# Performance work log

Measured on AMD Instinct MI355X. Metric: run time of the kernel, lower is better.

Reference implementation:

```python
import jax, jax.numpy as jnp
import numpy as np

L = 2; B = 16; H = 56; W = 56; N = H * W; D = 256
HEADS = 8; HD = 32; INNER = HEADS * HD
WIN = 7; WIN2 = WIN * WIN; NWH = H // WIN; NWW = W // WIN; NW = NWH * NWW
DISP = WIN // 2; FF = 4 * D; CPB = 512; EPS = 1e-5


def _shift_masks():
    d = DISP
    ul = np.zeros((WIN2, WIN2), np.float32)
    ul[-d * WIN:, :-d * WIN] = -np.inf
    ul[:-d * WIN, -d * WIN:] = -np.inf
    lr = np.zeros((WIN, WIN, WIN, WIN), np.float32)
    lr[:, -d:, :, :-d] = -np.inf
    lr[:, :-d, :, -d:] = -np.inf
    return jnp.asarray(ul), jnp.asarray(lr.reshape(WIN2, WIN2))

MASK_UL, MASK_LR = _shift_masks()

_idx = np.array([[i, j] for i in range(WIN) for j in range(WIN)], np.float32)
_rel = _idx[None, :, :] - _idx[:, None, :]  # (49,49,2) relative distances
REL = jnp.asarray((np.sign(_rel) * np.log1p(np.abs(_rel))).reshape(WIN2 * WIN2, 2))


def _ln(x, g, b):
    m = x.mean(-1, keepdims=True)
    v = ((x - m) ** 2).mean(-1, keepdims=True)
    return (x - m) / jnp.sqrt(v + EPS) * g + b


def _l2norm(t):
    return t / jnp.maximum(jnp.linalg.norm(t, axis=-1, keepdims=True), 1e-12)


def _window_attn(xm, qkv_w, tau, cw1, cb1, cw2, cb2, ow, ob, shifted):
    if shifted:
        xm = jnp.roll(xm, (-DISP, -DISP), (1, 2))
    qkv = xm @ qkv_w  # (B,H,W,3*INNER), no bias
    q, k, v = jnp.split(qkv, 3, axis=-1)

    def towin(t):  # (B,H,W,INNER) -> (B,heads,nw,win2,hd)
        t = t.reshape(B, NWH, WIN, NWW, WIN, HEADS, HD)
        return t.transpose(0, 5, 1, 3, 2, 4, 6).reshape(B, HEADS, NW, WIN2, HD)

    q, k, v = towin(q), towin(k), towin(v)
    # cosine-similarity attention
    dots = jnp.einsum('bhwid,bhwjd->bhwij', _l2norm(q), _l2norm(k))
    dots = dots / jnp.clip(tau, 0.01, None)[None, :, None, None, None]
    # continuous position bias MLP: 2 -> CPB -> heads
    cpb = (jax.nn.relu(REL @ cw1 + cb1) @ cw2 + cb2).reshape(WIN2, WIN2, HEADS)
    dots = dots + cpb.transpose(2, 0, 1)[None, :, None]
    if shifted:
        dots = dots.at[:, :, -NWW:].add(MASK_UL)
        dots = dots.at[:, :, NWW - 1::NWW].add(MASK_LR)
    attn = jax.nn.softmax(dots, -1)
    out = jnp.einsum('bhwij,bhwjd->bhwid', attn, v)
    out = out.reshape(B, HEADS, NWH, NWW, WIN, WIN, HD)
    out = out.transpose(0, 2, 4, 3, 5, 1, 6).reshape(B, H, W, INNER)
    out = out @ ow + ob
    if shifted:
        out = jnp.roll(out, (DISP, DISP), (1, 2))
    return out


def _forward(x, spe, qkv_w, tau, cw1, cb1, cw2, cb2, ow, ob, ln1_g, ln1_b,
             fw1, fb1, fw2, fb2, ln2_g, ln2_b, norm_g, norm_b):
    xm = (x + spe).reshape(B, H, W, D)
    for i in range(L):
        shifted = (i % 2 == 1)
        a = _window_attn(xm, qkv_w[i], tau[i], cw1[i], cb1[i], cw2[i], cb2[i],
                         ow[i], ob[i], shifted)
        xm = _ln(a, ln1_g[i], ln1_b[i]) + xm  # Residual(PostNorm(attn))
        f = jax.nn.gelu(xm @ fw1[i] + fb1[i], approximate=False) @ fw2[i] + fb2[i]
        xm = _ln(f, ln2_g[i], ln2_b[i]) + xm  # Residual(PostNorm(mlp))
    return _ln(xm, norm_g, norm_b).reshape(B, N, D)


def setup_inputs():
    key = jax.random.key(0)
    ks = jax.random.split(key, 10)
    rn = lambda k, shp, s: jax.random.normal(k, shp, jnp.float32) * s
    return {
        'x': rn(ks[0], (B, N, D), 1.0),
        'spatial_position_embedding': rn(ks[1], (B, N, D), 0.02),
        'qkv_w': rn(ks[2], (L, D, 3 * INNER), 0.02),
        'tau': jnp.ones((L, HEADS), jnp.float32),
        'cw1': rn(ks[3], (L, 2, CPB), 0.1),
        'cb1': jnp.zeros((L, CPB), jnp.float32),
        'cw2': rn(ks[4], (L, CPB, HEADS), 0.05),
        'cb2': jnp.zeros((L, HEADS), jnp.float32),
        'ow': rn(ks[5], (L, INNER, D), 0.02),
        'ob': jnp.zeros((L, D), jnp.float32),
        'ln1_g': jnp.ones((L, D), jnp.float32),
        'ln1_b': jnp.zeros((L, D), jnp.float32),
        'fw1': rn(ks[6], (L, D, FF), 0.02),
        'fb1': jnp.zeros((L, FF), jnp.float32),
        'fw2': rn(ks[7], (L, FF, D), 0.02),
        'fb2': jnp.zeros((L, D), jnp.float32),
        'ln2_g': jnp.ones((L, D), jnp.float32),
        'ln2_b': jnp.zeros((L, D), jnp.float32),
        'norm_g': jnp.ones((D,), jnp.float32),
        'norm_b': jnp.zeros((D,), jnp.float32),
    }


def reference(x, spatial_position_embedding, qkv_w, tau, cw1, cb1, cw2, cb2, ow, ob,
              ln1_g, ln1_b, fw1, fb1, fw2, fb2, ln2_g, ln2_b, norm_g, norm_b):
    return _forward(x, spatial_position_embedding, qkv_w, tau, cw1, cb1, cw2, cb2,
                    ow, ob, ln1_g, ln1_b, fw1, fb1, fw2, fb2, ln2_g, ln2_b,
                    norm_g, norm_b)
```

## Files before the change

kernel.cpp:

```cpp
#include <hip/hip_runtime.h>
#include <hip/hip_bf16.h>
#include <math.h>

typedef short    short8  __attribute__((ext_vector_type(8)));
typedef float    floatx4 __attribute__((ext_vector_type(4)));

__device__ __forceinline__ float b2f(unsigned short u) {
    union { float f; unsigned int i; } v; v.i = ((unsigned int)u) << 16; return v.f;
}
__device__ __forceinline__ unsigned short f2b(float f) {
    union { float f; unsigned int i; } v; v.f = f;
    unsigned int b = v.i;
    return (unsigned short)((b + 0x7FFFu + ((b >> 16) & 1u)) >> 16);
}
__device__ __forceinline__ float rd(const void* p, long i, int f) {
    return f ? ((const float*)p)[i] : b2f(((const unsigned short*)p)[i]);
}
__device__ __forceinline__ float fgelu(float x) {
    float u = 0.7978845608f * x * (1.f + 0.044715f * x * x);
    float e = __expf(-2.f * fabsf(u));
    float th = 1.f - 2.f * e / (1.f + e);
    th = (u < 0.f) ? -th : th;
    return 0.5f * x * (1.f + th);
}

#define NTOK_ 50176

__global__ __launch_bounds__(256) void k_detect(const unsigned short* __restrict__ x,
                                                int* __restrict__ flag) {
    __shared__ int cnt;
    if (threadIdx.x == 0) cnt = 0;
    __syncthreads();
    unsigned short v = x[threadIdx.x];
    int e = (v >> 7) & 0xFF;
    if (e >= 0x90) atomicAdd(&cnt, 1);
    __syncthreads();
    if (threadIdx.x == 0) *flag = (cnt >= 8) ? 1 : 0;
}

__global__ __launch_bounds__(256) void k_add_spe(const void* __restrict__ x,
                                                 const void* __restrict__ spe,
                                                 float* __restrict__ xm,
                                                 const int* __restrict__ flagp) {
    const int f = *flagp;
    long i = ((long)blockIdx.x * 256 + threadIdx.x) * 4;
    float4 o;
    if (f) {
        float4 a = *(const float4*)((const float*)x + i);
        float4 b = *(const float4*)((const float*)spe + i);
        o.x = a.x + b.x; o.y = a.y + b.y; o.z = a.z + b.z; o.w = a.w + b.w;
    } else {
        ushort4 a = *(const ushort4*)((const unsigned short*)x + i);
        ushort4 b = *(const ushort4*)((const unsigned short*)spe + i);
        o.x = b2f(a.x) + b2f(b.x); o.y = b2f(a.y) + b2f(b.y);
        o.z = b2f(a.z) + b2f(b.z); o.w = b2f(a.w) + b2f(b.w);
    }
    *(float4*)(xm + i) = o;
}

__global__ __launch_bounds__(256) void k_transpose(const void* __restrict__ in, long ioff,
                                                   unsigned short* __restrict__ out,
                                                   int K, int N,
                                                   const int* __restrict__ flagp) {
    const int f = *flagp;
    int i = blockIdx.x * 256 + threadIdx.x;
    if (i >= K * N) return;
    int k = i / N, n = i - k * N;
    unsigned short o;
    if (f) o = f2b(((const float*)in)[ioff + i]);
    else   o = ((const unsigned short*)in)[ioff + i];
    out[(long)n * K + k] = o;
}

__global__ __launch_bounds__(512) void k_cpb(const void* __restrict__ cw1,
                                             const void* __restrict__ cb1,
                                             const void* __restrict__ cw2,
                                             const void* __restrict__ cb2,
                                             float* __restrict__ cpb,
                                             const int* __restrict__ flagp) {
    const int f = *flagp;
    int p = blockIdx.x;
    int l = blockIdx.y;
    int t = threadIdx.x;
    int i = p / 49, j = p - i * 49;
    int yi = i / 7, xi = i - yi * 7, yj = j / 7, xj = j - yj * 7;
    float dy = (float)(yj - yi), dx = (float)(xj - xi);
    float sy = (dy > 0.f) ? 1.f : ((dy < 0.f) ? -1.f : 0.f);
    float sx = (dx > 0.f) ? 1.f : ((dx < 0.f) ? -1.f : 0.f);
    float r0 = sy * log1pf(fabsf(dy));
    float r1 = sx * log1pf(fabsf(dx));
    float h = r0 * rd(cw1, l * 1024 + t, f) + r1 * rd(cw1, l * 1024 + 512 + t, f)
            + rd(cb1, l * 512 + t, f);
    h = fmaxf(h, 0.f);
    __shared__ float red[512];
    for (int hh = 0; hh < 8; hh++) {
        red[t] = h * rd(cw2, (long)(l * 512 + t) * 8 + hh, f);
        __syncthreads();
        for (int s = 256; s > 0; s >>= 1) {
            if (t < s) red[t] += red[t + s];
            __syncthreads();
        }
        if (t == 0) cpb[((long)l * 8 + hh) * 2401 + p] = red[0] + rd(cb2, l * 8 + hh, f);
        __syncthreads();
    }
}

__global__ __launch_bounds__(256) void k_cast_roll(const float* __restrict__ xmg,
                                                   unsigned short* __restrict__ xb, int shift) {
    int gid = blockIdx.x * 256 + threadIdx.x;
    int c4 = (gid & 63) * 4;
    int t = gid >> 6;
    int x = t % 56; int t2 = t / 56;
    int y = t2 % 56;
    int b = t2 / 56;
    int ys = y + shift; if (ys >= 56) ys -= 56;
    int xs = x + shift; if (xs >= 56) xs -= 56;
    float4 v = *(const float4*)(xmg + (((long)b * 3136 + ys * 56 + xs) * 256 + c4));
    ushort4 o; o.x = f2b(v.x); o.y = f2b(v.y); o.z = f2b(v.z); o.w = f2b(v.w);
    *(ushort4*)(xb + ((long)t * 256 + c4)) = o;
}

__global__ __launch_bounds__(256) void gemm_bt(const unsigned short* __restrict__ A,
                                               const unsigned short* __restrict__ Bt,
                                               const void* __restrict__ bias, long boff,
                                               void* __restrict__ Cp,
                                               int M, int N, int K, int flags,
                                               const int* __restrict__ flagp) {
    __shared__ __align__(16) unsigned short smem[16896];
    unsigned short* As = smem;
    unsigned short* Bs = smem + 5120;
    const int f = *flagp;
    const int tid = threadIdx.x;
    const int lane = tid & 63;
    const int wave = tid >> 6;
    const int wrow = (wave >> 1) * 64;
    const int wcol = (wave & 1) * 64;
    const int bm = blockIdx.x, bn = blockIdx.y;

    floatx4 acc[4][4] = {};

    const int arow = tid >> 2;
    const int aseg = (tid & 3) * 8;
    const unsigned short* Ag = A + (long)(bm * 128 + arow) * K + aseg;
    const unsigned short* Bg = Bt + (long)(bn * 128 + arow) * K + aseg;
    const long arow2 = (long)64 * K;

    const int q = lane >> 4;
    const int mrow = lane & 15;

    for (int k0 = 0; k0 < K; k0 += 32) {
        uint4 a0 = *(const uint4*)(Ag + k0);
        uint4 a1 = *(const uint4*)(Ag + k0 + arow2);
        uint4 b0 = *(const uint4*)(Bg + k0);
        uint4 b1 = *(const uint4*)(Bg + k0 + arow2);
        __syncthreads();
        *(uint4*)(As + arow * 40 + aseg) = a0;
        *(uint4*)(As + (arow + 64) * 40 + aseg) = a1;
        *(uint4*)(Bs + arow * 40 + aseg) = b0;
        *(uint4*)(Bs + (arow + 64) * 40 + aseg) = b1;
        __syncthreads();

        short8 af_[4], bf_[4];
#pragma unroll
        for (int mt = 0; mt < 4; mt++)
            af_[mt] = *(const short8*)(As + (wrow + mt * 16 + mrow) * 40 + q * 8);
#pragma unroll
        for (int nt = 0; nt < 4; nt++)
            bf_[nt] = *(const short8*)(Bs + (wcol + nt * 16 + mrow) * 40 + q * 8);
#pragma unroll
        for (int mt = 0; mt < 4; mt++)
#pragma unroll
            for (int nt = 0; nt < 4; nt++)
                acc[mt][nt] = __builtin_amdgcn_mfma_f32_16x16x32_bf16(af_[mt], bf_[nt], acc[mt][nt], 0, 0, 0);
    }

    __syncthreads();

    if (flags & 4) {
        unsigned short* T = smem;
#pragma unroll
        for (int nt = 0; nt < 4; nt++) {
            int col = wcol + nt * 16 + mrow;
            float bv = (flags & 1) ? rd(bias, boff + bn * 128 + col, f) : 0.f;
#pragma unroll
            for (int mt = 0; mt < 4; mt++) {
                int row0 = wrow + mt * 16 + q * 4;
#pragma unroll
                for (int r = 0; r < 4; r++) {
                    float v = acc[mt][nt][r] + bv;
                    if (flags & 2) v = fgelu(v);
                    T[(row0 + r) * 132 + col] = f2b(v);
                }
            }
        }
        __syncthreads();
        unsigned short* Cu = (unsigned short*)Cp;
        int row = tid >> 4;
        int col8 = (tid & 15) * 8;
#pragma unroll
        for (int p = 0; p < 8; p++) {
            int rr = p * 16 + row;
            *(uint4*)(Cu + (long)(bm * 128 + rr) * N + bn * 128 + col8) =
                *(const uint4*)(T + rr * 132 + col8);
        }
    } else {
        float* Tf = (float*)smem;
        float* Cf = (float*)Cp;
        float bvc[4];
#pragma unroll
        for (int nt = 0; nt < 4; nt++)
            bvc[nt] = (flags & 1) ? rd(bias, boff + bn * 128 + wcol + nt * 16 + mrow, f) : 0.f;
        int row = tid >> 5;
        int col4 = (tid & 31) * 4;
#pragma unroll
        for (int half = 0; half < 2; half++) {
            if (half) __syncthreads();
            if (wrow == half * 64) {
#pragma unroll
                for (int nt = 0; nt < 4; nt++) {
                    int col = wcol + nt * 16 + mrow;
#pragma unroll
                    for (int mt = 0; mt < 4; mt++) {
                        int lrow0 = mt * 16 + q * 4;
#pragma unroll
                        for (int r = 0; r < 4; r++) {
                            float v = acc[mt][nt][r] + bvc[nt];
                            if (flags & 2) v = fgelu(v);
                            Tf[(lrow0 + r) * 132 + col] = v;
                        }
                    }
                }
            }
            __syncthreads();
#pragma unroll
            for (int p = 0; p < 8; p++) {
                int rr = p * 8 + row;
                *(float4*)(Cf + (long)(bm * 128 + half * 64 + rr) * N + bn * 128 + col4) =
                    *(const float4*)(Tf + rr * 132 + col4);
            }
        }
    }
}

__global__ __launch_bounds__(256) void gemm_ln(const unsigned short* __restrict__ A,
                                               const unsigned short* __restrict__ Bt,
                                               const void* __restrict__ bias, long boff,
                                               const void* __restrict__ g, long goff,
                                               const void* __restrict__ bb, long b2off,
                                               float* __restrict__ xm,
                                               unsigned short* __restrict__ xb,
                                               int K,
                                               const int* __restrict__ flagp) {
    __shared__ __align__(16) unsigned short smem[17152];
    __shared__ float pp[4][64][2];
    unsigned short* As = smem;
    unsigned short* Bs = smem + 2560;
    const int f = *flagp;
    const int tid = threadIdx.x;
    const int lane = tid & 63;
    const int wv = tid >> 6;
    const int wcol = wv * 64;
    const int bm = blockIdx.x;

    floatx4 acc[4][4] = {};
    const int arow = tid >> 2;
    const int aseg = (tid & 3) * 8;
    const unsigned short* Ag = A + (long)(bm * 64 + arow) * K + aseg;
    const unsigned short* Bg = Bt + (long)arow * K + aseg;
    const long brow2 = (long)64 * K;
    const int q = lane >> 4;
    const int c = lane & 15;

    for (int k0 = 0; k0 < K; k0 += 32) {
        uint4 a0 = *(const uint4*)(Ag + k0);
        uint4 b0 = *(const uint4*)(Bg + k0);
        uint4 b1 = *(const uint4*)(Bg + k0 + brow2);
        uint4 b2 = *(const uint4*)(Bg + k0 + 2 * brow2);
        uint4 b3 = *(const uint4*)(Bg + k0 + 3 * brow2);
        __syncthreads();
        *(uint4*)(As + arow * 40 + aseg) = a0;
        *(uint4*)(Bs + arow * 40 + aseg) = b0;
        *(uint4*)(Bs + (arow + 64) * 40 + aseg) = b1;
        *(uint4*)(Bs + (arow + 128) * 40 + aseg) = b2;
        *(uint4*)(Bs + (arow + 192) * 40 + aseg) = b3;
        __syncthreads();

        short8 af_[4], bf_[4];
#pragma unroll
        for (int mt = 0; mt < 4; mt++)
            af_[mt] = *(const short8*)(As + (mt * 16 + c) * 40 + q * 8);
#pragma unroll
        for (int nt = 0; nt < 4; nt++)
            bf_[nt] = *(const short8*)(Bs + (wcol + nt * 16 + c) * 40 + q * 8);
#pragma unroll
        for (int mt = 0; mt < 4; mt++)
#pragma unroll
            for (int nt = 0; nt < 4; nt++)
                acc[mt][nt] = __builtin_amdgcn_mfma_f32_16x16x32_bf16(af_[mt], bf_[nt], acc[mt][nt], 0, 0, 0);
    }
    __syncthreads();

    float bv[4];
#pragma unroll
    for (int nt = 0; nt < 4; nt++)
        bv[nt] = rd(bias, boff + wcol + nt * 16 + c, f);
#pragma unroll
    for (int mt = 0; mt < 4; mt++) {
#pragma unroll
        for (int r = 0; r < 4; r++) {
            float s1 = 0.f, s2 = 0.f;
#pragma unroll
            for (int nt = 0; nt < 4; nt++) {
                float v = acc[mt][nt][r] + bv[nt];
                s1 += v; s2 += v * v;
            }
            s1 += __shfl_xor(s1, 1); s2 += __shfl_xor(s2, 1);
            s1 += __shfl_xor(s1, 2); s2 += __shfl_xor(s2, 2);
            s1 += __shfl_xor(s1, 4); s2 += __shfl_xor(s2, 4);
            s1 += __shfl_xor(s1, 8); s2 += __shfl_xor(s2, 8);
            if (c == 0) {
                pp[wv][mt * 16 + q * 4 + r][0] = s1;
                pp[wv][mt * 16 + q * 4 + r][1] = s2;
            }
        }
    }

    const int c0 = lane * 4;
    float4 gv, bbv;
    gv.x = rd(g, goff + c0 + 0, f); gv.y = rd(g, goff + c0 + 1, f);
    gv.z = rd(g, goff + c0 + 2, f); gv.w = rd(g, goff + c0 + 3, f);
    bbv.x = rd(bb, b2off + c0 + 0, f); bbv.y = rd(bb, b2off + c0 + 1, f);
    bbv.z = rd(bb, b2off + c0 + 2, f); bbv.w = rd(bb, b2off + c0 + 3, f);
    __syncthreads();

    float* Tf = (float*)smem;
#pragma unroll
    for (int half = 0; half < 2; half++) {
        if (half) __syncthreads();
#pragma unroll
        for (int mt2 = 0; mt2 < 2; mt2++) {
            int mt = half * 2 + mt2;
#pragma unroll
            for (int nt = 0; nt < 4; nt++)
#pragma unroll
                for (int r = 0; r < 4; r++)
                    Tf[(mt2 * 16 + q * 4 + r) * 268 + wcol + nt * 16 + c] = acc[mt][nt][r] + bv[nt];
        }
        __syncthreads();
#pragma unroll
        for (int it = 0; it < 8; it++) {
            int lr = wv * 8 + it;
            int row = half * 32 + lr;
            float sum = pp[0][row][0] + pp[1][row][0] + pp[2][row][0] + pp[3][row][0];
            float ssq = pp[0][row][1] + pp[1][row][1] + pp[2][row][1] + pp[3][row][1];
            float mean = sum * (1.f / 256.f);
            float var = ssq * (1.f / 256.f) - mean * mean;
            float rstd = rsqrtf(fmaxf(var, 0.f) + 1e-5f);
            long grow = (long)(bm * 64 + row) * 256;
            float4 t = *(const float4*)(Tf + lr * 268 + c0);
            float4 xv = *(const float4*)(xm + grow + c0);
            float4 o;
            o.x = (t.x - mean) * rstd * gv.x + bbv.x + xv.x;
            o.y = (t.y - mean) * rstd * gv.y + bbv.y + xv.y;
            o.z = (t.z - mean) * rstd * gv.z + bbv.z + xv.z;
            o.w = (t.w - mean) * rstd * gv.w + bbv.w + xv.w;
            *(float4*)(xm + grow + c0) = o;
            ushort4 hb; hb.x = f2b(o.x); hb.y = f2b(o.y); hb.z = f2b(o.z); hb.w = f2b(o.w);
            *(ushort4*)(xb + grow + c0) = hb;
        }
    }
}

__global__ __launch_bounds__(256) void k_attn(const unsigned short* __restrict__ qkv,
                                              const float* __restrict__ cpb,
                                              const void* __restrict__ tau, long toff,
                                              unsigned short* __restrict__ out,
                                              int shifted,
                                              const int* __restrict__ flagp) {
    __shared__ __align__(16) unsigned short Pbuf[4][64 * 72];
    __shared__ __align__(16) unsigned short Vt[4][32 * 72];
    __shared__ float inq_s[4][64], ink_s[4][64];

    const int f = *flagp;
    const int tid = threadIdx.x;
    const int wv = tid >> 6;
    const int lane = tid & 63;
    const int h = blockIdx.x * 4 + wv;
    const int w = blockIdx.y, b = blockIdx.z;
    const int wy = w >> 3, wx = w & 7;
    const int q = lane >> 4;
    const int c = lane & 15;

    short8 qa[4], kb[4];
    float sqv[4], skv[4];
#pragma unroll
    for (int mt = 0; mt < 4; mt++) {
        int i = mt * 16 + c; if (i > 48) i = 48;
        int py = i / 7, px = i - py * 7;
        long base = (((long)b * 56 + wy * 7 + py) * 56 + wx * 7 + px) * 768 + h * 32 + q * 8;
        qa[mt] = *(const short8*)(qkv + base);
        kb[mt] = *(const short8*)(qkv + base + 256);
        float sq = 0.f, sk = 0.f;
#pragma unroll
        for (int e = 0; e < 8; e++) {
            float a = b2f((unsigned short)qa[mt][e]); sq += a * a;
            float k2 = b2f((unsigned short)kb[mt][e]); sk += k2 * k2;
        }
        sqv[mt] = sq; skv[mt] = sk;
    }
#pragma unroll
    for (int mt = 0; mt < 4; mt++) {
        float sq = sqv[mt]; sq += __shfl_xor(sq, 16); sq += __shfl_xor(sq, 32);
        float sk = skv[mt]; sk += __shfl_xor(sk, 16); sk += __shfl_xor(sk, 32);
        if (q == 0) {
            inq_s[wv][mt * 16 + c] = 1.f / fmaxf(sqrtf(sq), 1e-12f);
            ink_s[wv][mt * 16 + c] = 1.f / fmaxf(sqrtf(sk), 1e-12f);
        }
    }

    floatx4 acc[4][4] = {};
#pragma unroll
    for (int mt = 0; mt < 4; mt++)
#pragma unroll
        for (int nt = 0; nt < 4; nt++)
            acc[mt][nt] = __builtin_amdgcn_mfma_f32_16x16x32_bf16(qa[mt], kb[nt], acc[mt][nt], 0, 0, 0);

#pragma unroll
    for (int z = lane; z < 576; z += 64)
        *(uint2*)(&Vt[wv][z * 4]) = make_uint2(0u, 0u);
    if (lane < 49) {
        int py = lane / 7, px = lane - py * 7;
        long base = (((long)b * 56 + wy * 7 + py) * 56 + wx * 7 + px) * 768 + h * 32 + 512;
#pragma unroll
        for (int dd = 0; dd < 32; dd += 8) {
            ushort4 v0 = *(const ushort4*)(qkv + base + dd);
            ushort4 v1 = *(const ushort4*)(qkv + base + dd + 4);
            Vt[wv][(dd + 0) * 72 + lane] = v0.x;
            Vt[wv][(dd + 1) * 72 + lane] = v0.y;
            Vt[wv][(dd + 2) * 72 + lane] = v0.z;
            Vt[wv][(dd + 3) * 72 + lane] = v0.w;
            Vt[wv][(dd + 4) * 72 + lane] = v1.x;
            Vt[wv][(dd + 5) * 72 + lane] = v1.y;
            Vt[wv][(dd + 6) * 72 + lane] = v1.z;
            Vt[wv][(dd + 7) * 72 + lane] = v1.w;
        }
    }

    float scale = 1.f / fmaxf(rd(tau, toff + h, f), 0.01f);
#pragma unroll
    for (int mt = 0; mt < 4; mt++) {
#pragma unroll
        for (int r = 0; r < 4; r++) {
            int i = mt * 16 + q * 4 + r;
            int ci = (i < 49) ? i : 48;
            int pyi = ci / 7, pxi = ci - pyi * 7;
            float qi = inq_s[wv][ci] * scale;
            float vals[4];
#pragma unroll
            for (int nt = 0; nt < 4; nt++) {
                int j = nt * 16 + c;
                if (j < 49) {
                    float v = acc[mt][nt][r] * qi * ink_s[wv][j]
                            + cpb[h * 2401 + ci * 49 + j];
                    if (shifted) {
                        int pyj = j / 7, pxj = j - pyj * 7;
                        if (wy == 7 && ((pyi >= 4) != (pyj >= 4))) v = -1e30f;
                        if (wx == 7 && ((pxi >= 4) != (pxj >= 4))) v = -1e30f;
                    }
                    vals[nt] = v;
                } else vals[nt] = -1e30f;
            }
            float m = fmaxf(fmaxf(vals[0], vals[1]), fmaxf(vals[2], vals[3]));
            m = fmaxf(m, __shfl_xor(m, 1)); m = fmaxf(m, __shfl_xor(m, 2));
            m = fmaxf(m, __shfl_xor(m, 4)); m = fmaxf(m, __shfl_xor(m, 8));
            float s = 0.f;
#pragma unroll
            for (int nt = 0; nt < 4; nt++) { vals[nt] = __expf(vals[nt] - m); s += vals[nt]; }
            s += __shfl_xor(s, 1); s += __shfl_xor(s, 2);
            s += __shfl_xor(s, 4); s += __shfl_xor(s, 8);
            float rinv = 1.f / s;
#pragma unroll
            for (int nt = 0; nt < 4; nt++)
                Pbuf[wv][i * 72 + nt * 16 + c] = f2b(vals[nt] * rinv);
        }
    }

    floatx4 accO[4][2] = {};
#pragma unroll
    for (int ks = 0; ks < 2; ks++) {
        short8 pa[4], vb[2];
#pragma unroll
        for (int mt = 0; mt < 4; mt++)
            pa[mt] = *(const short8*)(&Pbuf[wv][(mt * 16 + c) * 72 + ks * 32 + q * 8]);
#pragma unroll
        for (int nt = 0; nt < 2; nt++)
            vb[nt] = *(const short8*)(&Vt[wv][(nt * 16 + c) * 72 + ks * 32 + q * 8]);
#pragma unroll
        for (int mt = 0; mt < 4; mt++)
#pragma unroll
            for (int nt = 0; nt < 2; nt++)
                accO[mt][nt] = __builtin_amdgcn_mfma_f32_16x16x32_bf16(pa[mt], vb[nt], accO[mt][nt], 0, 0, 0);
    }

    int sh = shifted ? 3 : 0;
#pragma unroll
    for (int mt = 0; mt < 4; mt++) {
#pragma unroll
        for (int r = 0; r < 4; r++) {
            int i = mt * 16 + q * 4 + r;
            if (i < 49) {
                int py = i / 7, px = i - py * 7;
                int yo = wy * 7 + py + sh; if (yo >= 56) yo -= 56;
                int xo = wx * 7 + px + sh; if (xo >= 56) xo -= 56;
                long ob = (((long)b * 56 + yo) * 56 + xo) * 256 + h * 32;
                out[ob + c]      = f2b(accO[mt][0][r]);
                out[ob + 16 + c] = f2b(accO[mt][1][r]);
            }
        }
    }
}

__global__ __launch_bounds__(256) void k_final(const float* __restrict__ xm,
                                               const void* __restrict__ g,
                                               const void* __restrict__ bb,
                                               void* __restrict__ out,
                                               const int* __restrict__ flagp) {
    const int f = *flagp;
    int t = blockIdx.x, c = threadIdx.x;
    long off = (long)t * 256 + c;
    float v = xm[off];
    __shared__ float red[256];
    red[c] = v; __syncthreads();
#pragma unroll
    for (int s = 128; s > 0; s >>= 1) {
        if (c < s) red[c] += red[c + s];
        __syncthreads();
    }
    float mean = red[0] * (1.f / 256.f);
    __syncthreads();
    float d = v - mean;
    red[c] = d * d; __syncthreads();
#pragma unroll
    for (int s = 128; s > 0; s >>= 1) {
        if (c < s) red[c] += red[c + s];
        __syncthreads();
    }
    float var = red[0] * (1.f / 256.f);
    float ln = d * rsqrtf(var + 1e-5f) * rd(g, c, f) + rd(bb, c, f);
    if (f) ((float*)out)[off] = ln;
    else   ((unsigned short*)out)[off] = f2b(ln);
}

extern "C" void kernel_launch(void* const* d_in, const int* in_sizes, int n_in,
                              void* d_out, int out_size, void* d_ws, size_t ws_size,
                              hipStream_t stream) {
    char* ws = (char*)d_ws;
    float*          xm    = (float*)(ws + 0);
    unsigned short* wt    = (unsigned short*)(ws + 51380224);
    float*          cpb   = (float*)(ws + 54525952);
    int*            flagp = (int*)(ws + 54679616);
    const size_t DYN = 54680576;

    long Mg = NTOK_; int G = 1;
    while (G <= 8) {
        Mg = NTOK_ / G;
        if (DYN + (size_t)Mg * 2560 <= ws_size) break;
        G <<= 1;
    }
    if (G > 8) { G = 8; Mg = NTOK_ / 8; }
    const int NB = 16 / G;

    unsigned short* xb   = (unsigned short*)(ws + DYN);
    unsigned short* qkvb = (unsigned short*)(ws + DYN + Mg * 512);
    unsigned short* hid  = (unsigned short*)(ws + DYN + Mg * 512);

    k_detect<<<1, 256, 0, stream>>>((const unsigned short*)d_in[0], flagp);

    for (int l = 0; l < 2; l++) {
        unsigned short* base = wt + (long)l * 786432;
        k_transpose<<<dim3(768), 256, 0, stream>>>(d_in[2],  (long)l * 196608, base,          256, 768,  flagp);
        k_transpose<<<dim3(256), 256, 0, stream>>>(d_in[8],  (long)l * 65536,  base + 196608, 256, 256,  flagp);
        k_transpose<<<dim3(1024), 256, 0, stream>>>(d_in[12], (long)l * 262144, base + 262144, 256, 1024, flagp);
        k_transpose<<<dim3(1024), 256, 0, stream>>>(d_in[14], (long)l * 262144, base + 524288, 1024, 256, flagp);
    }
    k_cpb<<<dim3(2401, 2), 512, 0, stream>>>(d_in[4], d_in[5], d_in[6], d_in[7], cpb, flagp);
    k_add_spe<<<dim3(12544), 256, 0, stream>>>(d_in[0], d_in[1], xm, flagp);

    for (int l = 0; l < 2; l++) {
        int sh = (l & 1) ? 3 : 0;
        unsigned short* base = wt + (long)l * 786432;
        for (int g = 0; g < G; g++) {
            long m0 = (long)g * Mg;
            k_cast_roll<<<dim3(Mg / 4), 256, 0, stream>>>(xm + m0 * 256, xb, sh);
            gemm_bt<<<dim3(Mg / 128, 6), 256, 0, stream>>>(xb, base, nullptr, 0, qkvb,
                                                           (int)Mg, 768, 256, 4, flagp);
            k_attn<<<dim3(2, 64, NB), 256, 0, stream>>>(qkvb, cpb + (long)l * 19208,
                                                        d_in[3], (long)l * 8, xb, (l & 1), flagp);
            gemm_ln<<<dim3(Mg / 64), 256, 0, stream>>>(xb, base + 196608, d_in[9], (long)l * 256,
                                                       d_in[10], (long)l * 256, d_in[11], (long)l * 256,
                                                       xm + m0 * 256, xb, 256, flagp);
            gemm_bt<<<dim3(Mg / 128, 8), 256, 0, stream>>>(xb, base + 262144, d_in[13], (long)l * 1024,
                                                           hid, (int)Mg, 1024, 256, 1 | 2 | 4, flagp);
            gemm_ln<<<dim3(Mg / 64), 256, 0, stream>>>(hid, base + 524288, d_in[15], (long)l * 256,
                                                       d_in[16], (long)l * 256, d_in[17], (long)l * 256,
                                                       xm + m0 * 256, xb, 1024, flagp);
        }
    }
    k_final<<<dim3(NTOK_), 256, 0, stream>>>(xm, d_in[18], d_in[19], d_out, flagp);
}
```

Before: 980.1 us.

## Use direct global-to-LDS loads in GEMMs, fuse cast/roll into epilogues, tile transposes

The GEMM mainloops now use global_load_lds to copy A/B tiles straight into LDS without a register round trip, with an unpadded 32-element row stride. When the whole batch fits in workspace, the separate cast/roll kernel is dropped: add_spe writes the bf16 copy and the second LN epilogue writes the rolled bf16 tensor for the next layer. Weight transposes use an LDS-tiled kernel, and the GEMM grid is reordered so N-blocks vary fastest for A-tile reuse. The unpadded LDS layout may add bank conflicts on fragment reads, and the global_load_lds layout must match the per-wave lane mapping.

```diff
diff --git a/kernel.cpp b/kernel.cpp
--- a/kernel.cpp
+++ b/kernel.cpp
@@ -22,6 +22,11 @@
     float th = 1.f - 2.f * e / (1.f + e);
     th = (u < 0.f) ? -th : th;
     return 0.5f * x * (1.f + th);
+}
+__device__ __forceinline__ void gl_lds16(const unsigned short* g, unsigned short* l) {
+    __builtin_amdgcn_global_load_lds(
+        (const __attribute__((address_space(1))) void*)g,
+        (__attribute__((address_space(3))) void*)l, 16, 0, 0);
 }
 
 #define NTOK_ 50176
@@ -41,6 +46,7 @@
 __global__ __launch_bounds__(256) void k_add_spe(const void* __restrict__ x,
                                                  const void* __restrict__ spe,
                                                  float* __restrict__ xm,
+                                                 unsigned short* __restrict__ xb,
                                                  const int* __restrict__ flagp) {
     const int f = *flagp;
     long i = ((long)blockIdx.x * 256 + threadIdx.x) * 4;
@@ -56,20 +62,34 @@
         o.z = b2f(a.z) + b2f(b.z); o.w = b2f(a.w) + b2f(b.w);
     }
     *(float4*)(xm + i) = o;
+    if (xb) {
+        ushort4 h; h.x = f2b(o.x); h.y = f2b(o.y); h.z = f2b(o.z); h.w = f2b(o.w);
+        *(ushort4*)(xb + i) = h;
+    }
 }
 
 __global__ __launch_bounds__(256) void k_transpose(const void* __restrict__ in, long ioff,
                                                    unsigned short* __restrict__ out,
                                                    int K, int N,
                                                    const int* __restrict__ flagp) {
+    __shared__ unsigned short tile[32][33];
     const int f = *flagp;
-    int i = blockIdx.x * 256 + threadIdx.x;
-    if (i >= K * N) return;
-    int k = i / N, n = i - k * N;
-    unsigned short o;
-    if (f) o = f2b(((const float*)in)[ioff + i]);
-    else   o = ((const unsigned short*)in)[ioff + i];
-    out[(long)n * K + k] = o;
+    int n0 = blockIdx.x * 32, k0 = blockIdx.y * 32;
+    int tx = threadIdx.x & 31, ty = threadIdx.x >> 5;
+#pragma unroll
+    for (int i = 0; i < 4; i++) {
+        int k = k0 + ty + i * 8;
+        long idx = ioff + (long)k * N + n0 + tx;
+        unsigned short v = f ? f2b(((const float*)in)[idx])
+                             : ((const unsigned short*)in)[idx];
+        tile[ty + i * 8][tx] = v;
+    }
+    __syncthreads();
+#pragma unroll
+    for (int i = 0; i < 4; i++) {
+        int n = n0 + ty + i * 8;
+        out[(long)n * K + k0 + tx] = tile[tx][ty + i * 8];
+    }
 }
 
 __global__ __launch_bounds__(512) void k_cpb(const void* __restrict__ cw1,
@@ -128,45 +148,43 @@
                                                const int* __restrict__ flagp) {
     __shared__ __align__(16) unsigned short smem[16896];
     unsigned short* As = smem;
-    unsigned short* Bs = smem + 5120;
+    unsigned short* Bs = smem + 4096;
     const int f = *flagp;
     const int tid = threadIdx.x;
     const int lane = tid & 63;
     const int wave = tid >> 6;
     const int wrow = (wave >> 1) * 64;
     const int wcol = (wave & 1) * 64;
-    const int bm = blockIdx.x, bn = blockIdx.y;
+    const int bn = blockIdx.x, bm = blockIdx.y;
 
     floatx4 acc[4][4] = {};
 
-    const int arow = tid >> 2;
-    const int aseg = (tid & 3) * 8;
-    const unsigned short* Ag = A + (long)(bm * 128 + arow) * K + aseg;
-    const unsigned short* Bg = Bt + (long)(bn * 128 + arow) * K + aseg;
-    const long arow2 = (long)64 * K;
+    const int trow = tid >> 2;
+    const int tseg = (tid & 3) * 8;
+    const unsigned short* Ag = A + (long)(bm * 128 + trow) * K + tseg;
+    const unsigned short* Bg = Bt + (long)(bn * 128 + trow) * K + tseg;
+    const long rstep = (long)64 * K;
+    unsigned short* Asw = As + wave * 512;
+    unsigned short* Bsw = Bs + wave * 512;
 
     const int q = lane >> 4;
     const int mrow = lane & 15;
 
     for (int k0 = 0; k0 < K; k0 += 32) {
-        uint4 a0 = *(const uint4*)(Ag + k0);
-        uint4 a1 = *(const uint4*)(Ag + k0 + arow2);
-        uint4 b0 = *(const uint4*)(Bg + k0);
-        uint4 b1 = *(const uint4*)(Bg + k0 + arow2);
-        __syncthreads();
-        *(uint4*)(As + arow * 40 + aseg) = a0;
-        *(uint4*)(As + (arow + 64) * 40 + aseg) = a1;
-        *(uint4*)(Bs + arow * 40 + aseg) = b0;
-        *(uint4*)(Bs + (arow + 64) * 40 + aseg) = b1;
+        __syncthreads();
+        gl_lds16(Ag + k0, Asw);
+        gl_lds16(Ag + k0 + rstep, Asw + 2048);
+        gl_lds16(Bg + k0, Bsw);
+        gl_lds16(Bg + k0 + rstep, Bsw + 2048);
         __syncthreads();
 
         short8 af_[4], bf_[4];
 #pragma unroll
         for (int mt = 0; mt < 4; mt++)
-            af_[mt] = *(const short8*)(As + (wrow + mt * 16 + mrow) * 40 + q * 8);
+            af_[mt] = *(const short8*)(As + (wrow + mt * 16 + mrow) * 32 + q * 8);
 #pragma unroll
         for (int nt = 0; nt < 4; nt++)
-            bf_[nt] = *(const short8*)(Bs + (wcol + nt * 16 + mrow) * 40 + q * 8);
+            bf_[nt] = *(const short8*)(Bs + (wcol + nt * 16 + mrow) * 32 + q * 8);
 #pragma unroll
         for (int mt = 0; mt < 4; mt++)
 #pragma unroll
@@ -249,12 +267,12 @@
                                                const void* __restrict__ bb, long b2off,
                                                float* __restrict__ xm,
                                                unsigned short* __restrict__ xb,
-                                               int K,
+                                               int K, int xbmode,
                                                const int* __restrict__ flagp) {
     __shared__ __align__(16) unsigned short smem[17152];
     __shared__ float pp[4][64][2];
     unsigned short* As = smem;
-    unsigned short* Bs = smem + 2560;
+    unsigned short* Bs = smem + 2048;
     const int f = *flagp;
     const int tid = threadIdx.x;
     const int lane = tid & 63;
@@ -263,35 +281,32 @@
     const int bm = blockIdx.x;
 
     floatx4 acc[4][4] = {};
-    const int arow = tid >> 2;
-    const int aseg = (tid & 3) * 8;
-    const unsigned short* Ag = A + (long)(bm * 64 + arow) * K + aseg;
-    const unsigned short* Bg = Bt + (long)arow * K + aseg;
-    const long brow2 = (long)64 * K;
+    const int trow = tid >> 2;
+    const int tseg = (tid & 3) * 8;
+    const unsigned short* Ag = A + (long)(bm * 64 + trow) * K + tseg;
+    const unsigned short* Bg = Bt + (long)trow * K + tseg;
+    const long rstep = (long)64 * K;
+    unsigned short* Asw = As + wv * 512;
+    unsigned short* Bsw = Bs + wv * 512;
     const int q = lane >> 4;
     const int c = lane & 15;
 
     for (int k0 = 0; k0 < K; k0 += 32) {
-        uint4 a0 = *(const uint4*)(Ag + k0);
-        uint4 b0 = *(const uint4*)(Bg + k0);
-        uint4 b1 = *(const uint4*)(Bg + k0 + brow2);
-        uint4 b2 = *(const uint4*)(Bg + k0 + 2 * brow2);
-        uint4 b3 = *(const uint4*)(Bg + k0 + 3 * brow2);
-        __syncthreads();
-        *(uint4*)(As + arow * 40 + aseg) = a0;
-        *(uint4*)(Bs + arow * 40 + aseg) = b0;
-        *(uint4*)(Bs + (arow + 64) * 40 + aseg) = b1;
-        *(uint4*)(Bs + (arow + 128) * 40 + aseg) = b2;
-        *(uint4*)(Bs + (arow + 192) * 40 + aseg) = b3;
+        __syncthreads();
+        gl_lds16(Ag + k0, Asw);
+        gl_lds16(Bg + k0, Bsw);
+        gl_lds16(Bg + k0 + rstep, Bsw + 2048);
+        gl_lds16(Bg + k0 + 2 * rstep, Bsw + 4096);
+        gl_lds16(Bg + k0 + 3 * rstep, Bsw + 6144);
         __syncthreads();
 
         short8 af_[4], bf_[4];
 #pragma unroll
         for (int mt = 0; mt < 4; mt++)
-            af_[mt] = *(const short8*)(As + (mt * 16 + c) * 40 + q * 8);
+            af_[mt] = *(const short8*)(As + (mt * 16 + c) * 32 + q * 8);
 #pragma unroll
         for (int nt = 0; nt < 4; nt++)
-            bf_[nt] = *(const short8*)(Bs + (wcol + nt * 16 + c) * 40 + q * 8);
+            bf_[nt] = *(const short8*)(Bs + (wcol + nt * 16 + c) * 32 + q * 8);
 #pragma unroll
         for (int mt = 0; mt < 4; mt++)
 #pragma unroll
@@ -356,7 +371,8 @@
             float mean = sum * (1.f / 256.f);
             float var = ssq * (1.f / 256.f) - mean * mean;
             float rstd = rsqrtf(fmaxf(var, 0.f) + 1e-5f);
-            long grow = (long)(bm * 64 + row) * 256;
+            long tok = (long)(bm * 64 + row);
+            long grow = tok * 256;
             float4 t = *(const float4*)(Tf + lr * 268 + c0);
             float4 xv = *(const float4*)(xm + grow + c0);
             float4 o;
@@ -365,8 +381,18 @@
             o.z = (t.z - mean) * rstd * gv.z + bbv.z + xv.z;
             o.w = (t.w - mean) * rstd * gv.w + bbv.w + xv.w;
             *(float4*)(xm + grow + c0) = o;
-            ushort4 hb; hb.x = f2b(o.x); hb.y = f2b(o.y); hb.z = f2b(o.z); hb.w = f2b(o.w);
-            *(ushort4*)(xb + grow + c0) = hb;
+            if (xbmode) {
+                long xg = grow;
+                if (xbmode == 2) {
+                    int bi = (int)(tok / 3136); int r2 = (int)(tok - (long)bi * 3136);
+                    int y = r2 / 56; int x = r2 - y * 56;
+                    y = (y >= 3) ? y - 3 : y + 53;
+                    x = (x >= 3) ? x - 3 : x + 53;
+                    xg = ((long)bi * 3136 + y * 56 + x) * 256;
+                }
+                ushort4 hb; hb.x = f2b(o.x); hb.y = f2b(o.y); hb.z = f2b(o.z); hb.w = f2b(o.w);
+                *(ushort4*)(xb + xg + c0) = hb;
+            }
         }
     }
 }
@@ -569,6 +595,7 @@
     }
     if (G > 8) { G = 8; Mg = NTOK_ / 8; }
     const int NB = 16 / G;
+    const bool fused = (G == 1);
 
     unsigned short* xb   = (unsigned short*)(ws + DYN);
     unsigned short* qkvb = (unsigned short*)(ws + DYN + Mg * 512);
@@ -578,32 +605,35 @@
 
     for (int l = 0; l < 2; l++) {
         unsigned short* base = wt + (long)l * 786432;
-        k_transpose<<<dim3(768), 256, 0, stream>>>(d_in[2],  (long)l * 196608, base,          256, 768,  flagp);
-        k_transpose<<<dim3(256), 256, 0, stream>>>(d_in[8],  (long)l * 65536,  base + 196608, 256, 256,  flagp);
-        k_transpose<<<dim3(1024), 256, 0, stream>>>(d_in[12], (long)l * 262144, base + 262144, 256, 1024, flagp);
-        k_transpose<<<dim3(1024), 256, 0, stream>>>(d_in[14], (long)l * 262144, base + 524288, 1024, 256, flagp);
+        k_transpose<<<dim3(24, 8), 256, 0, stream>>>(d_in[2],  (long)l * 196608, base,          256, 768,  flagp);
+        k_transpose<<<dim3(8, 8),  256, 0, stream>>>(d_in[8],  (long)l * 65536,  base + 196608, 256, 256,  flagp);
+        k_transpose<<<dim3(32, 8), 256, 0, stream>>>(d_in[12], (long)l * 262144, base + 262144, 256, 1024, flagp);
+        k_transpose<<<dim3(8, 32), 256, 0, stream>>>(d_in[14], (long)l * 262144, base + 524288, 1024, 256, flagp);
     }
     k_cpb<<<dim3(2401, 2), 512, 0, stream>>>(d_in[4], d_in[5], d_in[6], d_in[7], cpb, flagp);
-    k_add_spe<<<dim3(12544), 256, 0, stream>>>(d_in[0], d_in[1], xm, flagp);
+    k_add_spe<<<dim3(12544), 256, 0, stream>>>(d_in[0], d_in[1], xm,
+                                               fused ? xb : (unsigned short*)nullptr, flagp);
 
     for (int l = 0; l < 2; l++) {
         int sh = (l & 1) ? 3 : 0;
         unsigned short* base = wt + (long)l * 786432;
         for (int g = 0; g < G; g++) {
             long m0 = (long)g * Mg;
-            k_cast_roll<<<dim3(Mg / 4), 256, 0, stream>>>(xm + m0 * 256, xb, sh);
-            gemm_bt<<<dim3(Mg / 128, 6), 256, 0, stream>>>(xb, base, nullptr, 0, qkvb,
+            if (!fused)
+                k_cast_roll<<<dim3(Mg / 4), 256, 0, stream>>>(xm + m0 * 256, xb, sh);
+            gemm_bt<<<dim3(6, Mg / 128), 256, 0, stream>>>(xb, base, nullptr, 0, qkvb,
                                                            (int)Mg, 768, 256, 4, flagp);
             k_attn<<<dim3(2, 64, NB), 256, 0, stream>>>(qkvb, cpb + (long)l * 19208,
                                                         d_in[3], (long)l * 8, xb, (l & 1), flagp);
             gemm_ln<<<dim3(Mg / 64), 256, 0, stream>>>(xb, base + 196608, d_in[9], (long)l * 256,
                                                        d_in[10], (long)l * 256, d_in[11], (long)l * 256,
-                                                       xm + m0 * 256, xb, 256, flagp);
-            gemm_bt<<<dim3(Mg / 128, 8), 256, 0, stream>>>(xb, base + 262144, d_in[13], (long)l * 1024,
+                                                       xm + m0 * 256, xb, 256, 1, flagp);
+            gemm_bt<<<dim3(8, Mg / 128), 256, 0, stream>>>(xb, base + 262144, d_in[13], (long)l * 1024,
                                                            hid, (int)Mg, 1024, 256, 1 | 2 | 4, flagp);
+            int xbm = fused ? ((l == 0) ? 2 : 0) : 1;
             gemm_ln<<<dim3(Mg / 64), 256, 0, stream>>>(hid, base + 524288, d_in[15], (long)l * 256,
                                                        d_in[16], (long)l * 256, d_in[17], (long)l * 256,
-                                                       xm + m0 * 256, xb, 1024, flagp);
+                                                       xm + m0 * 256, xb, 1024, xbm, flagp);
         }
     }
     k_final<<<dim3(NTOK_), 256, 0, stream>>>(xm, d_in[18], d_in[19], d_out, flagp);
```

Measured after the change: 965.5 us. About the same (-1.5%).
